# Kernel tuning notes

Hardware: AMD Instinct MI355X
Metric: run time of the kernel (lower is better)

Reference implementation:

```python
import jax, jax.numpy as jnp
import numpy as np

OBS_DIM = 512
ACT_DIM = 32
HIDDEN_DIM = 1024
MSG_DIM = 128
POS_EM_DIM = 128
T = 256


def pos_table(n, dim):
    pos = np.arange(n)[:, None].astype(np.float64)
    j = np.arange(dim)[None, :]
    tab = pos / np.power(10000.0, 2 * (j // 2) / dim)
    tab[:, 0::2] = np.sin(tab[:, 0::2])
    tab[:, 1::2] = np.cos(tab[:, 1::2])
    return tab.astype(np.float32)


def setup_inputs() -> dict:
    key = jax.random.key(0)
    ks = jax.random.split(key, 12)
    in_dim = 1 + ACT_DIM
    s = 0.1
    return {
        "obs": jax.random.normal(ks[0], (T, OBS_DIM), jnp.float32),
        "prev_act": jax.random.normal(ks[1], (T, ACT_DIM), jnp.float32),
        "in_shift": jnp.zeros((OBS_DIM,), jnp.float32),
        "in_scale": jnp.ones((OBS_DIM,), jnp.float32),
        "pos_embedding": jnp.asarray(pos_table(HIDDEN_DIM, POS_EM_DIM)),
        "W_ih": s * jax.random.normal(ks[2], (4 * POS_EM_DIM, in_dim), jnp.float32),
        "b_ih": s * jax.random.normal(ks[3], (4 * POS_EM_DIM,), jnp.float32),
        "W_hh": s * jax.random.normal(ks[4], (4 * POS_EM_DIM, POS_EM_DIM), jnp.float32),
        "b_hh": s * jax.random.normal(ks[5], (4 * POS_EM_DIM,), jnp.float32),
        "Wq": s * jax.random.normal(ks[6], (MSG_DIM, POS_EM_DIM), jnp.float32),
        "bq": s * jax.random.normal(ks[7], (MSG_DIM,), jnp.float32),
        "Wk": s * jax.random.normal(ks[8], (MSG_DIM, POS_EM_DIM), jnp.float32),
        "bk": s * jax.random.normal(ks[9], (MSG_DIM,), jnp.float32),
    }


def reference(obs, prev_act, in_shift, in_scale, pos_embedding,
              W_ih, b_ih, W_hh, b_hh, Wq, bq, Wk, bk):
    # input normalization (buffers default to identity)
    x = (obs - in_shift) / (in_scale + 1e-8)  # (T, obs_dim)
    # query projection of the positional table is constant across steps
    q = pos_embedding @ Wq.T + bq             # (hidden_dim, msg_dim)
    inv_scale = 1.0 / jnp.sqrt(jnp.float32(MSG_DIM))

    def step(carry, inp):
        h, c = carry                            # (obs_dim, pos_em_dim) each
        s, a = inp                              # (obs_dim,), (act_dim,)
        # state-action pair: each obs scalar paired with the full prev action
        xa = jnp.concatenate(
            [s[:, None], jnp.broadcast_to(a, (OBS_DIM, ACT_DIM))], axis=-1)
        gates = xa @ W_ih.T + b_ih + h @ W_hh.T + b_hh
        i, f, g, o = jnp.split(gates, 4, axis=-1)  # torch LSTMCell gate order
        c = jax.nn.sigmoid(f) * c + jax.nn.sigmoid(i) * jnp.tanh(g)
        h = jax.nn.sigmoid(o) * jnp.tanh(c)
        k = h @ Wk.T + bk                       # (obs_dim, msg_dim)
        w = jnp.tanh((q @ k.T) * inv_scale)     # (hidden_dim, obs_dim)
        out = w @ s                             # (hidden_dim,)
        return (h, c), out

    h0 = jnp.zeros((OBS_DIM, POS_EM_DIM), x.dtype)
    c0 = jnp.zeros_like(h0)
    _, outs = jax.lax.scan(step, (h0, c0), (x, prev_act))
    return jnp.tanh(outs)                       # (T, hidden_dim)
```

## Files before the change

### kernel.cpp

```cpp
#include <hip/hip_runtime.h>
#include <hip/hip_fp16.h>

#define T_STEPS 256
#define OBS 512
#define ACT 32
#define HID 1024
#define PED 128
#define MSG 128
#define GATES 512
#define HSTR 136
#define KSTR 17
#define L1 1.4426950408889634f
#define L2C 2.8853900817779268f
#define QSCALE 0.2550348805576823f

typedef _Float16 half8  __attribute__((ext_vector_type(8)));
typedef float    floatx4 __attribute__((ext_vector_type(4)));

__device__ __forceinline__ float fast_exp2(float x) { return __builtin_amdgcn_exp2f(x); }
__device__ __forceinline__ float fast_rcp(float x)  { return __builtin_amdgcn_rcpf(x); }
__device__ __forceinline__ float tanh_f(float x) {
    return fmaf(-2.0f, fast_rcp(fast_exp2(2.8853900817779268f * x) + 1.0f), 1.0f);
}

__global__ void k_pre(const float* __restrict__ obs, const float* __restrict__ act,
                      const float* __restrict__ shift, const float* __restrict__ scale,
                      const float* __restrict__ W_ih, const float* __restrict__ b_ih,
                      const float* __restrict__ b_hh,
                      float* __restrict__ xnorm, float* __restrict__ apre_p) {
    int t = blockIdx.x;
    int tid = threadIdx.x;
    __shared__ float a_s[ACT];
    if (tid < ACT) a_s[tid] = act[t * ACT + tid];
    __syncthreads();
    for (int n = tid; n < OBS; n += 256) {
        xnorm[t * OBS + n] = (obs[t * OBS + n] - shift[n]) / (scale[n] + 1e-8f);
    }
    for (int j = tid; j < GATES; j += 256) {
        float acc = b_ih[j] + b_hh[j];
        const float* wr = W_ih + j * 33 + 1;
#pragma unroll
        for (int u = 0; u < ACT; ++u) acc = fmaf(a_s[u], wr[u], acc);
        int g = j >> 7, p = j & 127;
        apre_p[t * GATES + p * 4 + g] = acc;
    }
}

__global__ void k_qproj(const float* __restrict__ pe, const float* __restrict__ Wq,
                        const float* __restrict__ bq, const float* __restrict__ Wk,
                        const float* __restrict__ bk,
                        _Float16* __restrict__ qh, float* __restrict__ cb) {
    int m = blockIdx.x;
    int d = threadIdx.x;
    __shared__ float pe_s[PED];
    __shared__ float q_s[PED];
    __shared__ float red_s[2];
    pe_s[d] = pe[m * PED + d];
    __syncthreads();
    const float* wr = Wq + d * PED;
    float a = bq[d];
#pragma unroll 8
    for (int p = 0; p < PED; ++p) a = fmaf(pe_s[p], wr[p], a);
    q_s[d] = a;
    float pb = a * bk[d];
#pragma unroll
    for (int off = 32; off; off >>= 1) pb += __shfl_xor(pb, off, 64);
    if ((d & 63) == 0) red_s[d >> 6] = pb;
    __syncthreads();
    float acc = 0.f;
#pragma unroll 8
    for (int p = 0; p < PED; ++p) acc = fmaf(q_s[p], Wk[p * PED + d], acc);
    qh[m * PED + d] = (_Float16)(acc * QSCALE);
    if (d == 0) cb[m] = (red_s[0] + red_s[1]) * QSCALE;
}

__global__ __launch_bounds__(512, 1)
void k_lstm(const float* __restrict__ xnorm, const float* __restrict__ apre_p,
            const float* __restrict__ W_ih, const float* __restrict__ W_hh,
            _Float16* __restrict__ H16) {
    const int tid = threadIdx.x;
    const int lane = tid & 63, wv = tid >> 6;
    const int l15 = lane & 15, quad = lane >> 4;
    const int n0 = blockIdx.x * 4;
    const int p = 16 * wv + l15;

    half8 bfr[4][4];
    float wih0[4];
#pragma unroll
    for (int g = 0; g < 4; ++g) {
        const int col = 128 * g + p;
        const float* wrow = W_hh + (size_t)col * PED;
#pragma unroll
        for (int c = 0; c < 4; ++c) {
            const int k0 = c * 32 + quad * 8;
            float4 f0 = *(const float4*)(wrow + k0);
            float4 f1 = *(const float4*)(wrow + k0 + 4);
            bfr[g][c] = (half8){(_Float16)f0.x, (_Float16)f0.y, (_Float16)f0.z, (_Float16)f0.w,
                                (_Float16)f1.x, (_Float16)f1.y, (_Float16)f1.z, (_Float16)f1.w};
        }
        wih0[g] = W_ih[(size_t)col * 33];
    }

    __shared__ _Float16 h_s[2][16 * HSTR];
    __shared__ float x_s[T_STEPS * 4];

    for (int idx = tid; idx < T_STEPS * 4; idx += 512)
        x_s[idx] = xnorm[(idx >> 2) * OBS + n0 + (idx & 3)];
    for (int idx = tid; idx < 2 * 16 * HSTR; idx += 512)
        ((_Float16*)h_s)[idx] = (_Float16)0.f;

    float c0 = 0.f;
    const float* apl = apre_p + p * 4;
    float4 ap = *(const float4*)(apl);
    __syncthreads();

    _Float16* Hg = H16 + (size_t)(n0 + quad) * MSG + p;
    int buf = 0;
    for (int t = 0; t < T_STEPS; ++t) {
        half8 af[4];
        const _Float16* hb = h_s[buf] + l15 * HSTR + quad * 8;
#pragma unroll
        for (int c = 0; c < 4; ++c) af[c] = *(const half8*)(hb + c * 32);

        floatx4 acc[4];
        acc[0] = (floatx4){ap.x, ap.x, ap.x, ap.x};
        acc[1] = (floatx4){ap.y, ap.y, ap.y, ap.y};
        acc[2] = (floatx4){ap.z, ap.z, ap.z, ap.z};
        acc[3] = (floatx4){ap.w, ap.w, ap.w, ap.w};
#pragma unroll
        for (int g = 0; g < 4; ++g)
#pragma unroll
            for (int c = 0; c < 4; ++c)
                acc[g] = __builtin_amdgcn_mfma_f32_16x16x32_f16(
                    af[c], bfr[g][c], acc[g], 0, 0, 0);

        const int tn = (t + 1 < T_STEPS) ? t + 1 : t;
        float4 ap_n = *(const float4*)(apl + tn * GATES);

        const float x = x_s[t * 4 + quad];
        float gi = fmaf(x, wih0[0], acc[0][0]);
        float gf = fmaf(x, wih0[1], acc[1][0]);
        float gg = fmaf(x, wih0[2], acc[2][0]);
        float go = fmaf(x, wih0[3], acc[3][0]);

        float Di = 1.f + fast_exp2(fminf(-L1 * gi, 20.f));
        float Df = 1.f + fast_exp2(fminf(-L1 * gf, 20.f));
        float Dg = 1.f + fast_exp2(fminf(L2C * gg, 20.f));
        float DfDg = Df * Dg, DiDg = Di * Dg, DiDf = Di * Df;
        float r3 = fast_rcp(Di * DfDg);
        float iDi = r3 * DfDg, iDf = r3 * DiDg, iDg = r3 * DiDf;
        float cn = fmaf(iDf, c0, iDi * fmaf(-2.f, iDg, 1.f));
        c0 = cn;
        float Do = 1.f + fast_exp2(fminf(-L1 * go, 20.f));
        float Dc = 1.f + fast_exp2(fminf(L2C * cn, 20.f));
        float r2 = fast_rcp(Do * Dc);
        float iDo = r2 * Dc, iDc = r2 * Do;
        _Float16 hq = (_Float16)(iDo * fmaf(-2.f, iDc, 1.f));

        h_s[buf ^ 1][(4 * quad) * HSTR + p] = hq;
        Hg[0] = hq;
        Hg += OBS * MSG;

        ap = ap_n;
        buf ^= 1;
        __syncthreads();
    }
}

__global__ __launch_bounds__(256, 2)
void k_attn(const _Float16* __restrict__ qh, const float* __restrict__ cb,
            const _Float16* __restrict__ H16, const float* __restrict__ xnorm,
            float* __restrict__ outp) {
    const int t = blockIdx.x & 255;
    const int mq = blockIdx.x >> 8;
    const int tid = threadIdx.x;
    const int lane = tid & 63, wave = tid >> 6;
    const int l15 = lane & 15, quad = lane >> 4;
    const int m0 = mq * 128 + wave * 32;

    half8 afrag[2][4];
    floatx4 cbv[2];
#pragma unroll
    for (int mt = 0; mt < 2; ++mt) {
        const half8* qrow = (const half8*)(qh + (size_t)(m0 + mt * 16 + l15) * PED);
#pragma unroll
        for (int c = 0; c < 4; ++c) afrag[mt][c] = qrow[c * 4 + quad];
        cbv[mt] = *(const floatx4*)(cb + m0 + mt * 16 + quad * 4);
    }

    __shared__ half8 kbuf[2][64 * KSTR];

    float outacc[8];
#pragma unroll
    for (int i = 0; i < 8; ++i) outacc[i] = 0.f;

    const half8* Ht = (const half8*)(H16 + (size_t)t * (OBS * MSG));
    const float* xb = xnorm + t * OBS;

    half8 pf[4];
#pragma unroll
    for (int i = 0; i < 4; ++i) pf[i] = Ht[i * 256 + tid];
#pragma unroll
    for (int i = 0; i < 4; ++i) {
        int f = i * 256 + tid;
        kbuf[0][(f >> 4) * KSTR + (f & 15)] = pf[i];
    }
    __syncthreads();

    for (int ch = 0; ch < 8; ++ch) {
        const int cur = ch & 1;
        if (ch < 7) {
            const half8* Hn = Ht + (ch + 1) * 1024;
#pragma unroll
            for (int i = 0; i < 4; ++i) pf[i] = Hn[i * 256 + tid];
        }

#pragma unroll
        for (int nt = 0; nt < 4; ++nt) {
            half8 bfrag[4];
#pragma unroll
            for (int c = 0; c < 4; ++c)
                bfrag[c] = kbuf[cur][(nt * 16 + l15) * KSTR + c * 4 + quad];

            floatx4 acc[2];
#pragma unroll
            for (int mt = 0; mt < 2; ++mt) {
                acc[mt] = cbv[mt];
#pragma unroll
                for (int c = 0; c < 4; ++c)
                    acc[mt] = __builtin_amdgcn_mfma_f32_16x16x32_f16(
                        afrag[mt][c], bfrag[c], acc[mt], 0, 0, 0);
            }

            const float sv = xb[ch * 64 + nt * 16 + l15];
#pragma unroll
            for (int mt = 0; mt < 2; ++mt) {
                float E0 = fast_exp2(fminf(acc[mt][0], 20.f));
                float E1 = fast_exp2(fminf(acc[mt][1], 20.f));
                float E2 = fast_exp2(fminf(acc[mt][2], 20.f));
                float E3 = fast_exp2(fminf(acc[mt][3], 20.f));
                float D0 = 1.f + E0, D1 = 1.f + E1, D2 = 1.f + E2, D3 = 1.f + E3;
                float m01 = D0 * D1, m23 = D2 * D3;
                float rp = fast_rcp(m01 * m23);
                float rA = rp * m23, rB = rp * m01;
                float i0 = rA * D1, i1 = rA * D0, i2 = rB * D3, i3 = rB * D2;
                outacc[mt * 4 + 0] = fmaf(fmaf(-2.f, i0, 1.f), sv, outacc[mt * 4 + 0]);
                outacc[mt * 4 + 1] = fmaf(fmaf(-2.f, i1, 1.f), sv, outacc[mt * 4 + 1]);
                outacc[mt * 4 + 2] = fmaf(fmaf(-2.f, i2, 1.f), sv, outacc[mt * 4 + 2]);
                outacc[mt * 4 + 3] = fmaf(fmaf(-2.f, i3, 1.f), sv, outacc[mt * 4 + 3]);
            }
        }

        if (ch < 7) {
#pragma unroll
            for (int i = 0; i < 4; ++i) {
                int f = i * 256 + tid;
                kbuf[cur ^ 1][(f >> 4) * KSTR + (f & 15)] = pf[i];
            }
        }
        __syncthreads();
    }

#pragma unroll
    for (int i = 0; i < 8; ++i) {
        float v = outacc[i];
        v += __shfl_xor(v, 1, 16);
        v += __shfl_xor(v, 2, 16);
        v += __shfl_xor(v, 4, 16);
        v += __shfl_xor(v, 8, 16);
        outacc[i] = v;
    }
    if (l15 == 0) {
        const int mbase = m0 + quad * 4;
#pragma unroll
        for (int mt = 0; mt < 2; ++mt)
#pragma unroll
            for (int r = 0; r < 4; ++r)
                outp[(size_t)t * HID + mbase + mt * 16 + r] = tanh_f(outacc[mt * 4 + r]);
    }
}

extern "C" void kernel_launch(void* const* d_in, const int* in_sizes, int n_in,
                              void* d_out, int out_size, void* d_ws, size_t ws_size,
                              hipStream_t stream) {
    const float* obs      = (const float*)d_in[0];
    const float* prev_act = (const float*)d_in[1];
    const float* in_shift = (const float*)d_in[2];
    const float* in_scale = (const float*)d_in[3];
    const float* pos_emb  = (const float*)d_in[4];
    const float* W_ih     = (const float*)d_in[5];
    const float* b_ih     = (const float*)d_in[6];
    const float* W_hh     = (const float*)d_in[7];
    const float* b_hh     = (const float*)d_in[8];
    const float* Wq       = (const float*)d_in[9];
    const float* bq       = (const float*)d_in[10];
    const float* Wk       = (const float*)d_in[11];
    const float* bk       = (const float*)d_in[12];
    float* outp = (float*)d_out;

    float* ws = (float*)d_ws;
    float* xnorm  = ws;
    float* apre_p = ws + 131072;
    _Float16* qh  = (_Float16*)(ws + 262144);
    float* cbuf   = ws + 327680;
    _Float16* H16 = (_Float16*)(ws + 328704);

    k_pre<<<T_STEPS, 256, 0, stream>>>(obs, prev_act, in_shift, in_scale,
                                       W_ih, b_ih, b_hh, xnorm, apre_p);
    k_qproj<<<HID, 128, 0, stream>>>(pos_emb, Wq, bq, Wk, bk, qh, cbuf);
    k_lstm<<<128, 512, 0, stream>>>(xnorm, apre_p, W_ih, W_hh, H16);
    k_attn<<<T_STEPS * 8, 256, 0, stream>>>(qh, cbuf, H16, xnorm, outp);
}
```

Baseline: 302.5 us.

## Fuse LSTM and attention into producer-consumer kernel with flag-based synchronization

Merges the recurrent LSTM kernel and the attention kernel into one launch. 128 producer blocks run the recurrence and bump per-4-step atomic flags, while 128 consumer blocks spin on those flags and compute attention outputs for finished timesteps. This overlaps the attention work with the serial recurrence instead of running them back to back. In exchange, consumer blocks handle 2 timesteps each with less parallelism than the 2048-block attention grid, and correctness depends on all 256 blocks being co-resident on the device.

```diff
diff --git a/kernel.cpp b/kernel.cpp
--- a/kernel.cpp
+++ b/kernel.cpp
@@ -10,6 +10,8 @@
 #define GATES 512
 #define HSTR 136
 #define KSTR 17
+#define NPROD 128
+#define NCONS 128
 #define L1 1.4426950408889634f
 #define L2C 2.8853900817779268f
 #define QSCALE 0.2550348805576823f
@@ -27,9 +29,11 @@
                       const float* __restrict__ shift, const float* __restrict__ scale,
                       const float* __restrict__ W_ih, const float* __restrict__ b_ih,
                       const float* __restrict__ b_hh,
-                      float* __restrict__ xnorm, float* __restrict__ apre_p) {
+                      float* __restrict__ xnorm, float* __restrict__ apre_p,
+                      int* __restrict__ flags) {
     int t = blockIdx.x;
     int tid = threadIdx.x;
+    if (t == 0 && tid < 64) flags[tid] = 0;
     __shared__ float a_s[ACT];
     if (tid < ACT) a_s[tid] = act[t * ACT + tid];
     __syncthreads();
@@ -75,208 +79,231 @@
 }
 
 __global__ __launch_bounds__(512, 1)
-void k_lstm(const float* __restrict__ xnorm, const float* __restrict__ apre_p,
-            const float* __restrict__ W_ih, const float* __restrict__ W_hh,
-            _Float16* __restrict__ H16) {
+void k_fused(const float* __restrict__ xnorm, const float* __restrict__ apre_p,
+             const float* __restrict__ W_ih, const float* __restrict__ W_hh,
+             _Float16* __restrict__ H16, int* __restrict__ flags,
+             const _Float16* __restrict__ qh, const float* __restrict__ cb,
+             float* __restrict__ outp) {
+    __shared__ __align__(16) char smem[49152];
     const int tid = threadIdx.x;
-    const int lane = tid & 63, wv = tid >> 6;
+    const int lane = tid & 63;
     const int l15 = lane & 15, quad = lane >> 4;
-    const int n0 = blockIdx.x * 4;
-    const int p = 16 * wv + l15;
-
-    half8 bfr[4][4];
-    float wih0[4];
-#pragma unroll
-    for (int g = 0; g < 4; ++g) {
-        const int col = 128 * g + p;
-        const float* wrow = W_hh + (size_t)col * PED;
-#pragma unroll
-        for (int c = 0; c < 4; ++c) {
-            const int k0 = c * 32 + quad * 8;
-            float4 f0 = *(const float4*)(wrow + k0);
-            float4 f1 = *(const float4*)(wrow + k0 + 4);
-            bfr[g][c] = (half8){(_Float16)f0.x, (_Float16)f0.y, (_Float16)f0.z, (_Float16)f0.w,
-                                (_Float16)f1.x, (_Float16)f1.y, (_Float16)f1.z, (_Float16)f1.w};
+
+    if (blockIdx.x < NPROD) {
+        const int wv = tid >> 6;
+        const int n0 = blockIdx.x * 4;
+        const int p = 16 * wv + l15;
+
+        half8 bfr[4][4];
+        float wih0[4];
+#pragma unroll
+        for (int g = 0; g < 4; ++g) {
+            const int col = 128 * g + p;
+            const float* wrow = W_hh + (size_t)col * PED;
+#pragma unroll
+            for (int c = 0; c < 4; ++c) {
+                const int k0 = c * 32 + quad * 8;
+                float4 f0 = *(const float4*)(wrow + k0);
+                float4 f1 = *(const float4*)(wrow + k0 + 4);
+                bfr[g][c] = (half8){(_Float16)f0.x, (_Float16)f0.y, (_Float16)f0.z, (_Float16)f0.w,
+                                    (_Float16)f1.x, (_Float16)f1.y, (_Float16)f1.z, (_Float16)f1.w};
+            }
+            wih0[g] = W_ih[(size_t)col * 33];
         }
-        wih0[g] = W_ih[(size_t)col * 33];
-    }
-
-    __shared__ _Float16 h_s[2][16 * HSTR];
-    __shared__ float x_s[T_STEPS * 4];
-
-    for (int idx = tid; idx < T_STEPS * 4; idx += 512)
-        x_s[idx] = xnorm[(idx >> 2) * OBS + n0 + (idx & 3)];
-    for (int idx = tid; idx < 2 * 16 * HSTR; idx += 512)
-        ((_Float16*)h_s)[idx] = (_Float16)0.f;
-
-    float c0 = 0.f;
-    const float* apl = apre_p + p * 4;
-    float4 ap = *(const float4*)(apl);
-    __syncthreads();
-
-    _Float16* Hg = H16 + (size_t)(n0 + quad) * MSG + p;
-    int buf = 0;
-    for (int t = 0; t < T_STEPS; ++t) {
-        half8 af[4];
-        const _Float16* hb = h_s[buf] + l15 * HSTR + quad * 8;
-#pragma unroll
-        for (int c = 0; c < 4; ++c) af[c] = *(const half8*)(hb + c * 32);
-
-        floatx4 acc[4];
-        acc[0] = (floatx4){ap.x, ap.x, ap.x, ap.x};
-        acc[1] = (floatx4){ap.y, ap.y, ap.y, ap.y};
-        acc[2] = (floatx4){ap.z, ap.z, ap.z, ap.z};
-        acc[3] = (floatx4){ap.w, ap.w, ap.w, ap.w};
-#pragma unroll
-        for (int g = 0; g < 4; ++g)
-#pragma unroll
-            for (int c = 0; c < 4; ++c)
-                acc[g] = __builtin_amdgcn_mfma_f32_16x16x32_f16(
-                    af[c], bfr[g][c], acc[g], 0, 0, 0);
-
-        const int tn = (t + 1 < T_STEPS) ? t + 1 : t;
-        float4 ap_n = *(const float4*)(apl + tn * GATES);
-
-        const float x = x_s[t * 4 + quad];
-        float gi = fmaf(x, wih0[0], acc[0][0]);
-        float gf = fmaf(x, wih0[1], acc[1][0]);
-        float gg = fmaf(x, wih0[2], acc[2][0]);
-        float go = fmaf(x, wih0[3], acc[3][0]);
-
-        float Di = 1.f + fast_exp2(fminf(-L1 * gi, 20.f));
-        float Df = 1.f + fast_exp2(fminf(-L1 * gf, 20.f));
-        float Dg = 1.f + fast_exp2(fminf(L2C * gg, 20.f));
-        float DfDg = Df * Dg, DiDg = Di * Dg, DiDf = Di * Df;
-        float r3 = fast_rcp(Di * DfDg);
-        float iDi = r3 * DfDg, iDf = r3 * DiDg, iDg = r3 * DiDf;
-        float cn = fmaf(iDf, c0, iDi * fmaf(-2.f, iDg, 1.f));
-        c0 = cn;
-        float Do = 1.f + fast_exp2(fminf(-L1 * go, 20.f));
-        float Dc = 1.f + fast_exp2(fminf(L2C * cn, 20.f));
-        float r2 = fast_rcp(Do * Dc);
-        float iDo = r2 * Dc, iDc = r2 * Do;
-        _Float16 hq = (_Float16)(iDo * fmaf(-2.f, iDc, 1.f));
-
-        h_s[buf ^ 1][(4 * quad) * HSTR + p] = hq;
-        Hg[0] = hq;
-        Hg += OBS * MSG;
-
-        ap = ap_n;
-        buf ^= 1;
+
+        _Float16* h_s = (_Float16*)smem;
+        float* x_s = (float*)(smem + 2 * 16 * HSTR * 2);
+
+        for (int idx = tid; idx < T_STEPS * 4; idx += 512)
+            x_s[idx] = xnorm[(idx >> 2) * OBS + n0 + (idx & 3)];
+        for (int idx = tid; idx < 2 * 16 * HSTR; idx += 512)
+            h_s[idx] = (_Float16)0.f;
+
+        float c0 = 0.f;
+        const float* apl = apre_p + p * 4;
+        float4 ap = *(const float4*)(apl);
         __syncthreads();
-    }
-}
-
-__global__ __launch_bounds__(256, 2)
-void k_attn(const _Float16* __restrict__ qh, const float* __restrict__ cb,
-            const _Float16* __restrict__ H16, const float* __restrict__ xnorm,
-            float* __restrict__ outp) {
-    const int t = blockIdx.x & 255;
-    const int mq = blockIdx.x >> 8;
-    const int tid = threadIdx.x;
-    const int lane = tid & 63, wave = tid >> 6;
-    const int l15 = lane & 15, quad = lane >> 4;
-    const int m0 = mq * 128 + wave * 32;
-
-    half8 afrag[2][4];
-    floatx4 cbv[2];
-#pragma unroll
-    for (int mt = 0; mt < 2; ++mt) {
-        const half8* qrow = (const half8*)(qh + (size_t)(m0 + mt * 16 + l15) * PED);
-#pragma unroll
-        for (int c = 0; c < 4; ++c) afrag[mt][c] = qrow[c * 4 + quad];
-        cbv[mt] = *(const floatx4*)(cb + m0 + mt * 16 + quad * 4);
-    }
-
-    __shared__ half8 kbuf[2][64 * KSTR];
-
-    float outacc[8];
-#pragma unroll
-    for (int i = 0; i < 8; ++i) outacc[i] = 0.f;
-
-    const half8* Ht = (const half8*)(H16 + (size_t)t * (OBS * MSG));
-    const float* xb = xnorm + t * OBS;
-
-    half8 pf[4];
-#pragma unroll
-    for (int i = 0; i < 4; ++i) pf[i] = Ht[i * 256 + tid];
-#pragma unroll
-    for (int i = 0; i < 4; ++i) {
-        int f = i * 256 + tid;
-        kbuf[0][(f >> 4) * KSTR + (f & 15)] = pf[i];
-    }
-    __syncthreads();
-
-    for (int ch = 0; ch < 8; ++ch) {
-        const int cur = ch & 1;
-        if (ch < 7) {
-            const half8* Hn = Ht + (ch + 1) * 1024;
-#pragma unroll
-            for (int i = 0; i < 4; ++i) pf[i] = Hn[i * 256 + tid];
+
+        _Float16* Hg = H16 + (size_t)(n0 + quad) * MSG + p;
+        int buf = 0;
+        for (int t = 0; t < T_STEPS; ++t) {
+            half8 af[4];
+            const _Float16* hb = h_s + buf * (16 * HSTR) + l15 * HSTR + quad * 8;
+#pragma unroll
+            for (int c = 0; c < 4; ++c) af[c] = *(const half8*)(hb + c * 32);
+
+            floatx4 acc[4];
+            acc[0] = (floatx4){ap.x, ap.x, ap.x, ap.x};
+            acc[1] = (floatx4){ap.y, ap.y, ap.y, ap.y};
+            acc[2] = (floatx4){ap.z, ap.z, ap.z, ap.z};
+            acc[3] = (floatx4){ap.w, ap.w, ap.w, ap.w};
+#pragma unroll
+            for (int g = 0; g < 4; ++g)
+#pragma unroll
+                for (int c = 0; c < 4; ++c)
+                    acc[g] = __builtin_amdgcn_mfma_f32_16x16x32_f16(
+                        af[c], bfr[g][c], acc[g], 0, 0, 0);
+
+            const int tn = (t + 1 < T_STEPS) ? t + 1 : t;
+            float4 ap_n = *(const float4*)(apl + tn * GATES);
+
+            const float x = x_s[t * 4 + quad];
+            float gi = fmaf(x, wih0[0], acc[0][0]);
+            float gf = fmaf(x, wih0[1], acc[1][0]);
+            float gg = fmaf(x, wih0[2], acc[2][0]);
+            float go = fmaf(x, wih0[3], acc[3][0]);
+
+            float Di = 1.f + fast_exp2(fminf(-L1 * gi, 20.f));
+            float Df = 1.f + fast_exp2(fminf(-L1 * gf, 20.f));
+            float Dg = 1.f + fast_exp2(fminf(L2C * gg, 20.f));
+            float DfDg = Df * Dg, DiDg = Di * Dg, DiDf = Di * Df;
+            float r3 = fast_rcp(Di * DfDg);
+            float iDi = r3 * DfDg, iDf = r3 * DiDg, iDg = r3 * DiDf;
+            float cn = fmaf(iDf, c0, iDi * fmaf(-2.f, iDg, 1.f));
+            c0 = cn;
+            float Do = 1.f + fast_exp2(fminf(-L1 * go, 20.f));
+            float Dc = 1.f + fast_exp2(fminf(L2C * cn, 20.f));
+            float r2 = fast_rcp(Do * Dc);
+            float iDo = r2 * Dc, iDc = r2 * Do;
+            _Float16 hq = (_Float16)(iDo * fmaf(-2.f, iDc, 1.f));
+
+            h_s[(buf ^ 1) * (16 * HSTR) + (4 * quad) * HSTR + p] = hq;
+            Hg[0] = hq;
+            Hg += OBS * MSG;
+
+            ap = ap_n;
+            buf ^= 1;
+            __syncthreads();
+
+            if ((t & 3) == 3 && tid == 0)
+                __hip_atomic_fetch_add(&flags[t >> 2], 1, __ATOMIC_RELEASE,
+                                       __HIP_MEMORY_SCOPE_AGENT);
         }
-
-#pragma unroll
-        for (int nt = 0; nt < 4; ++nt) {
-            half8 bfrag[4];
-#pragma unroll
-            for (int c = 0; c < 4; ++c)
-                bfrag[c] = kbuf[cur][(nt * 16 + l15) * KSTR + c * 4 + quad];
-
-            floatx4 acc[2];
-#pragma unroll
-            for (int mt = 0; mt < 2; ++mt) {
-                acc[mt] = cbv[mt];
-#pragma unroll
-                for (int c = 0; c < 4; ++c)
-                    acc[mt] = __builtin_amdgcn_mfma_f32_16x16x32_f16(
-                        afrag[mt][c], bfrag[c], acc[mt], 0, 0, 0);
+    } else {
+        const int cidx = blockIdx.x - NPROD;
+        const int wave = tid >> 6;
+        half8* kbuf = (half8*)smem;
+
+        for (int pass = 0; pass < 2; ++pass) {
+            const int t = cidx * 2 + pass;
+
+            if (tid == 0) {
+                int it = 0;
+                while (__hip_atomic_fetch_add(&flags[t >> 2], 0, __ATOMIC_RELAXED,
+                                              __HIP_MEMORY_SCOPE_AGENT) < NPROD) {
+                    __builtin_amdgcn_s_sleep(32);
+                    if (++it > (1 << 22)) break;
+                }
+                __hip_atomic_fetch_add(&flags[t >> 2], 0, __ATOMIC_ACQUIRE,
+                                       __HIP_MEMORY_SCOPE_AGENT);
             }
-
-            const float sv = xb[ch * 64 + nt * 16 + l15];
-#pragma unroll
-            for (int mt = 0; mt < 2; ++mt) {
-                float E0 = fast_exp2(fminf(acc[mt][0], 20.f));
-                float E1 = fast_exp2(fminf(acc[mt][1], 20.f));
-                float E2 = fast_exp2(fminf(acc[mt][2], 20.f));
-                float E3 = fast_exp2(fminf(acc[mt][3], 20.f));
-                float D0 = 1.f + E0, D1 = 1.f + E1, D2 = 1.f + E2, D3 = 1.f + E3;
-                float m01 = D0 * D1, m23 = D2 * D3;
-                float rp = fast_rcp(m01 * m23);
-                float rA = rp * m23, rB = rp * m01;
-                float i0 = rA * D1, i1 = rA * D0, i2 = rB * D3, i3 = rB * D2;
-                outacc[mt * 4 + 0] = fmaf(fmaf(-2.f, i0, 1.f), sv, outacc[mt * 4 + 0]);
-                outacc[mt * 4 + 1] = fmaf(fmaf(-2.f, i1, 1.f), sv, outacc[mt * 4 + 1]);
-                outacc[mt * 4 + 2] = fmaf(fmaf(-2.f, i2, 1.f), sv, outacc[mt * 4 + 2]);
-                outacc[mt * 4 + 3] = fmaf(fmaf(-2.f, i3, 1.f), sv, outacc[mt * 4 + 3]);
+            __syncthreads();
+
+            const half8* Ht = (const half8*)(H16 + (size_t)t * (OBS * MSG));
+            const float* xb = xnorm + t * OBS;
+
+            for (int mq = 0; mq < 4; ++mq) {
+                const int m0 = mq * 256 + wave * 32;
+
+                half8 afrag[2][4];
+                floatx4 cbv[2];
+#pragma unroll
+                for (int mt = 0; mt < 2; ++mt) {
+                    const half8* qrow = (const half8*)(qh + (size_t)(m0 + mt * 16 + l15) * PED);
+#pragma unroll
+                    for (int c = 0; c < 4; ++c) afrag[mt][c] = qrow[c * 4 + quad];
+                    cbv[mt] = *(const floatx4*)(cb + m0 + mt * 16 + quad * 4);
+                }
+
+                float outacc[8];
+#pragma unroll
+                for (int i = 0; i < 8; ++i) outacc[i] = 0.f;
+
+                half8 pf[2];
+#pragma unroll
+                for (int i = 0; i < 2; ++i) pf[i] = Ht[i * 512 + tid];
+#pragma unroll
+                for (int i = 0; i < 2; ++i) {
+                    int f = i * 512 + tid;
+                    kbuf[(f >> 4) * KSTR + (f & 15)] = pf[i];
+                }
+                __syncthreads();
+
+                for (int ch = 0; ch < 8; ++ch) {
+                    const int cur = ch & 1;
+                    if (ch < 7) {
+                        const half8* Hn = Ht + (ch + 1) * 1024;
+#pragma unroll
+                        for (int i = 0; i < 2; ++i) pf[i] = Hn[i * 512 + tid];
+                    }
+
+#pragma unroll
+                    for (int nt = 0; nt < 4; ++nt) {
+                        half8 bfrag[4];
+#pragma unroll
+                        for (int c = 0; c < 4; ++c)
+                            bfrag[c] = kbuf[cur * (64 * KSTR) + (nt * 16 + l15) * KSTR + c * 4 + quad];
+
+                        floatx4 acc[2];
+#pragma unroll
+                        for (int mt = 0; mt < 2; ++mt) {
+                            acc[mt] = cbv[mt];
+#pragma unroll
+                            for (int c = 0; c < 4; ++c)
+                                acc[mt] = __builtin_amdgcn_mfma_f32_16x16x32_f16(
+                                    afrag[mt][c], bfrag[c], acc[mt], 0, 0, 0);
+                        }
+
+                        const float sv = xb[ch * 64 + nt * 16 + l15];
+#pragma unroll
+                        for (int mt = 0; mt < 2; ++mt) {
+                            float E0 = fast_exp2(fminf(acc[mt][0], 20.f));
+                            float E1 = fast_exp2(fminf(acc[mt][1], 20.f));
+                            float E2 = fast_exp2(fminf(acc[mt][2], 20.f));
+                            float E3 = fast_exp2(fminf(acc[mt][3], 20.f));
+                            float D0 = 1.f + E0, D1 = 1.f + E1, D2 = 1.f + E2, D3 = 1.f + E3;
+                            float m01 = D0 * D1, m23 = D2 * D3;
+                            float rp = fast_rcp(m01 * m23);
+                            float rA = rp * m23, rB = rp * m01;
+                            float i0 = rA * D1, i1 = rA * D0, i2 = rB * D3, i3 = rB * D2;
+                            outacc[mt * 4 + 0] = fmaf(fmaf(-2.f, i0, 1.f), sv, outacc[mt * 4 + 0]);
+                            outacc[mt * 4 + 1] = fmaf(fmaf(-2.f, i1, 1.f), sv, outacc[mt * 4 + 1]);
+                            outacc[mt * 4 + 2] = fmaf(fmaf(-2.f, i2, 1.f), sv, outacc[mt * 4 + 2]);
+                            outacc[mt * 4 + 3] = fmaf(fmaf(-2.f, i3, 1.f), sv, outacc[mt * 4 + 3]);
+                        }
+                    }
+
+                    if (ch < 7) {
+#pragma unroll
+                        for (int i = 0; i < 2; ++i) {
+                            int f = i * 512 + tid;
+                            kbuf[(cur ^ 1) * (64 * KSTR) + (f >> 4) * KSTR + (f & 15)] = pf[i];
+                        }
+                    }
+                    __syncthreads();
+                }
+
+#pragma unroll
+                for (int i = 0; i < 8; ++i) {
+                    float v = outacc[i];
+                    v += __shfl_xor(v, 1, 16);
+                    v += __shfl_xor(v, 2, 16);
+                    v += __shfl_xor(v, 4, 16);
+                    v += __shfl_xor(v, 8, 16);
+                    outacc[i] = v;
+                }
+                if (l15 == 0) {
+                    const int mbase = m0 + quad * 4;
+#pragma unroll
+                    for (int mt = 0; mt < 2; ++mt)
+#pragma unroll
+                        for (int r = 0; r < 4; ++r)
+                            outp[(size_t)t * HID + mbase + mt * 16 + r] =
+                                tanh_f(outacc[mt * 4 + r]);
+                }
+                __syncthreads();
             }
         }
-
-        if (ch < 7) {
-#pragma unroll
-            for (int i = 0; i < 4; ++i) {
-                int f = i * 256 + tid;
-                kbuf[cur ^ 1][(f >> 4) * KSTR + (f & 15)] = pf[i];
-            }
-        }
-        __syncthreads();
-    }
-
-#pragma unroll
-    for (int i = 0; i < 8; ++i) {
-        float v = outacc[i];
-        v += __shfl_xor(v, 1, 16);
-        v += __shfl_xor(v, 2, 16);
-        v += __shfl_xor(v, 4, 16);
-        v += __shfl_xor(v, 8, 16);
-        outacc[i] = v;
-    }
-    if (l15 == 0) {
-        const int mbase = m0 + quad * 4;
-#pragma unroll
-        for (int mt = 0; mt < 2; ++mt)
-#pragma unroll
-            for (int r = 0; r < 4; ++r)
-                outp[(size_t)t * HID + mbase + mt * 16 + r] = tanh_f(outacc[mt * 4 + r]);
     }
 }
 
@@ -303,11 +330,12 @@
     float* apre_p = ws + 131072;
     _Float16* qh  = (_Float16*)(ws + 262144);
     float* cbuf   = ws + 327680;
-    _Float16* H16 = (_Float16*)(ws + 328704);
+    int* flags    = (int*)(ws + 328704);
+    _Float16* H16 = (_Float16*)(ws + 328768);
 
     k_pre<<<T_STEPS, 256, 0, stream>>>(obs, prev_act, in_shift, in_scale,
-                                       W_ih, b_ih, b_hh, xnorm, apre_p);
+                                       W_ih, b_ih, b_hh, xnorm, apre_p, flags);
     k_qproj<<<HID, 128, 0, stream>>>(pos_emb, Wq, bq, Wk, bk, qh, cbuf);
-    k_lstm<<<128, 512, 0, stream>>>(xnorm, apre_p, W_ih, W_hh, H16);
-    k_attn<<<T_STEPS * 8, 256, 0, stream>>>(qh, cbuf, H16, xnorm, outp);
-}
+    k_fused<<<NPROD + NCONS, 512, 0, stream>>>(xnorm, apre_p, W_ih, W_hh,
+                                               H16, flags, qh, cbuf, outp);
+}
```

Result: slower. 736.3 us (+143.4%).
